# Performance work log

Measured on AMD Instinct MI355X. Metric: run time of the kernel, lower is better.

Reference implementation:

```python
import jax, jax.numpy as jnp
import numpy as np

NEG = -1.0e9
OBS_VOCAB = 64
Y_CLASSES = 32


def setup_inputs() -> dict:
    key = jax.random.key(0)
    ks = jax.random.split(key, 6)
    B, V, N, O, Y, HID = 256, 32, 8192, OBS_VOCAB, Y_CLASSES, 128
    tables = jax.random.randint(ks[0], (B, V, N), 0, O)
    sigma = jax.random.randint(ks[1], (B, N), 0, Y)
    x = jax.random.randint(ks[2], (B,), 0, N)
    base_obs = jax.random.randint(ks[3], (B,), 0, O)
    W1 = jax.random.normal(ks[4], (3, HID), dtype=jnp.float32) * 0.1
    b1 = jnp.zeros((HID,), dtype=jnp.float32)
    W2 = jax.random.normal(ks[5], (HID, 1), dtype=jnp.float32) * 0.1
    b2 = jnp.zeros((1,), dtype=jnp.float32)
    return {"tables": tables, "sigma": sigma, "x": x, "base_obs": base_obs,
            "W1": W1, "b1": b1, "W2": W2, "b2": b2, "max_steps": 8}


def reference(tables, sigma, x, base_obs, W1, b1, W2, b2, max_steps):
    B, V, N = tables.shape
    bidx = jnp.arange(B)
    vidx = jnp.arange(V)

    def step(carry, _):
        m, stopped, used = carry  # m: [B,N] candidate mask, used: [B,V]
        mf = m.astype(jnp.float32)
        total = jnp.maximum(mf.sum(-1), 1.0)  # [B]
        # oracle features: expected posterior set size after asking each view
        # counts[b,v,o] = #candidates in m whose tables[b,v,:] label is o
        counts = jnp.zeros((B, V, OBS_VOCAB), jnp.float32).at[
            bidx[:, None, None], vidx[None, :, None], tables].add(mf[:, None, :])
        gathered = jnp.take_along_axis(counts, tables, axis=-1)  # [B,V,N]
        exp_size = (gathered * mf[:, None, :]).sum(-1) / total[:, None]  # [B,V]
        steps_f = jnp.log2(jnp.maximum(exp_size, 1.0))
        amb_f = exp_size - 1.0
        feat_views = jnp.stack([steps_f, amb_f, exp_size], axis=-1)  # [B,V,3]
        feat_views = feat_views.at[:, 0, 0].set(1000.0)  # oracle cfg forbid_view0
        closed = total <= 1.0
        stop_steps = jnp.where(closed, 0.0, 1000.0)  # allow_stop_only_if_closed
        feat_stop = jnp.stack([stop_steps, total - 1.0, total], axis=-1)[:, None, :]
        feat = jnp.clip(jnp.concatenate([feat_views, feat_stop], axis=1), -1000.0, 1000.0)
        h = jax.nn.gelu(feat @ W1 + b1, approximate=False)
        z_logits = jax.lax.stop_gradient((h @ W2 + b2)[..., 0])  # [B,V+1] (detached)
        # straight-through z on detached logits reduces to a hard one-hot constant
        z = jax.nn.one_hot(jnp.argmax(z_logits, axis=-1), V + 1, dtype=jnp.float32)
        logits = z.at[:, 0].set(NEG)  # forbid view 0
        used_full = jnp.concatenate([used, jnp.zeros((B, 1), bool)], axis=1)
        logits = jnp.where(used_full, NEG, logits)  # mask already-used views
        a = jnp.argmax(logits, axis=-1)
        a = jnp.where(stopped, V, a)
        is_stop = a == V
        ac = jnp.clip(a, 0, V - 1)
        r = tables[bidx, ac, x]
        r = jnp.where(is_stop, 0, r)
        m_new = m & (is_stop[:, None] | (tables[bidx, ac, :] == r[:, None]))
        used_new = used.at[bidx, ac].set(True)
        return (m_new, stopped | is_stop, used_new), (a, r)

    m0 = tables[:, 0, :] == base_obs[:, None]
    carry0 = (m0, jnp.zeros((B,), bool), jnp.zeros((B, V), bool))
    (m, _, _), (a_seq, r_seq) = jax.lax.scan(step, carry0, None, length=int(max_steps))
    actions = a_seq.T  # [B, T]
    responses = r_seq.T
    # predict_y: exact constructive posterior over classes from candidate mask
    w = m.astype(jnp.float32)
    denom = jnp.maximum(w.sum(-1, keepdims=True), 1.0)
    state_dist = w / denom  # [B,N]
    p_sig = jnp.zeros((B, Y_CLASSES), jnp.float32).at[bidx[:, None], sigma].add(state_dist)
    y_logits = jnp.log(jnp.maximum(p_sig, 1e-9))
    return actions, responses, y_logits
```

## Files before the change

### kernel.cpp

```cpp
#include <hip/hip_runtime.h>
#include <math.h>

#define HP 65

__device__ __forceinline__ float clip1000(float v) {
  return fminf(fmaxf(v, -1000.0f), 1000.0f);
}

__device__ __noinline__ float mlp16(const float* w1a, const float* w1b,
                                    const float* w1c, const float* b1v,
                                    const float* w2v,
                                    float f0, float f1, float f2, int l) {
  float zp = 0.0f;
  {
    #pragma clang fp contract(off)
    #pragma clang loop unroll(disable)
    for (int k = l * 8; k < l * 8 + 8; ++k) {
      float pre = f0 * w1a[k] + f1 * w1b[k] + f2 * w1c[k] + b1v[k];
      float e = erff(pre / (float)M_SQRT2);
      float hg = 0.5f * pre * (1.0f + e);
      zp = zp + hg * w2v[k];
    }
  }
  zp += __shfl_xor(zp, 1);
  zp += __shfl_xor(zp, 2);
  zp += __shfl_xor(zp, 4);
  zp += __shfl_xor(zp, 8);
  return zp;
}

__launch_bounds__(1024, 1)
__global__ void sim_kernel(const int* __restrict__ tables,
                           const int* __restrict__ sigma,
                           const int* __restrict__ x,
                           const int* __restrict__ base_obs,
                           const float* __restrict__ W1,
                           const float* __restrict__ b1,
                           const float* __restrict__ W2,
                           const float* __restrict__ b2,
                           const int* __restrict__ max_steps_p,
                           float* __restrict__ out,
                           int B, int V, int N)
{
  const int b = blockIdx.x;
  const int tid = threadIdx.x;
  const int T = max_steps_p[0];

  __shared__ unsigned short s_pos[8192];
  __shared__ int s_gidx[8192];
  __shared__ int s_lab[256 * 33];
  __shared__ int s_h[2][32 * HP];
  __shared__ int s_surv[256];
  __shared__ float s_w1a[128], s_w1b[128], s_w1c[128], s_b1v[128], s_w2v[128];
  __shared__ float s_z[33];
  __shared__ float s_zc[6];
  __shared__ int s_used[32];
  __shared__ int s_ycnt[32];
  __shared__ int s_resp[32];
  __shared__ float s_b2v;
  __shared__ int s_nact, s_cnt, s_a, s_r;

  const int* tb = tables + (size_t)b * V * N;
  const int* sg = sigma + (size_t)b * N;
  const int bo = base_obs[b];
  const int xb = x[b];

  if (tid < 128) s_w1a[tid] = W1[tid];
  else if (tid < 256) s_w1b[tid - 128] = W1[tid];
  else if (tid < 384) s_w1c[tid - 256] = W1[tid];
  else if (tid < 512) s_b1v[tid - 384] = b1[tid - 384];
  else if (tid < 640) s_w2v[tid - 512] = W2[tid - 512];
  else if (tid == 640) s_b2v = b2[0];
  else if (tid >= 704 && tid < 736) s_resp[tid - 704] = tb[(size_t)(tid - 704) * N + xb];
  #pragma clang loop unroll(disable)
  for (int i = tid; i < 2 * 32 * HP; i += 1024) ((int*)s_h)[i] = 0;
  if (tid < 32) { s_used[tid] = 0; s_ycnt[tid] = 0; }
  if (tid == 0) s_nact = 0;
  __syncthreads();

  if (tid < 928) {
    const int4* tb4 = (const int4*)tb;
    #pragma clang loop unroll(disable)
    for (int q = tid; q < (N >> 2); q += 928) {
      int4 v4 = tb4[q]; int base = q << 2;
      if (v4.x == bo) { int p = atomicAdd(&s_nact, 1); s_gidx[p] = base; }
      if (v4.y == bo) { int p = atomicAdd(&s_nact, 1); s_gidx[p] = base + 1; }
      if (v4.z == bo) { int p = atomicAdd(&s_nact, 1); s_gidx[p] = base + 2; }
      if (v4.w == bo) { int p = atomicAdd(&s_nact, 1); s_gidx[p] = base + 3; }
    }
  } else {
    const int g = (tid - 928) >> 4, l = (tid - 928) & 15;
    const float zcf[6][3] = {
      {1.0f, 1.0f, 2.0f},
      {0.0f, 0.0f, 1.0f},
      {1000.0f, 0.0f, 1.0f},
      {1000.0f, 1.0f, 2.0f},
      {0.0f, -1.0f, 0.0f},
      {1000.0f, -1.0f, 0.0f}};
    if (g < 6) {
      float zp = mlp16(s_w1a, s_w1b, s_w1c, s_b1v, s_w2v,
                       zcf[g][0], zcf[g][1], zcf[g][2], l);
      if (l == 0) s_zc[g] = zp + s_b2v;
    }
  }
  __syncthreads();

  const int nact0 = s_nact;
  const bool cached = (nact0 <= 256);
  const int v32 = tid >> 5, g32 = tid & 31;

  auto labelOf = [&](int pos, int vv) -> int {
    return cached ? s_lab[pos * 33 + vv] : tb[(size_t)vv * N + s_gidx[pos]];
  };

  {
    const int* row = tb + (size_t)v32 * N;
    if (cached) {
      int labs[8];
      #pragma unroll
      for (int u = 0; u < 8; ++u) {
        int j = g32 + (u << 5);
        if (j < nact0) labs[u] = row[s_gidx[j]];
      }
      #pragma unroll
      for (int u = 0; u < 8; ++u) {
        int j = g32 + (u << 5);
        if (j < nact0) {
          s_lab[j * 33 + v32] = labs[u];
          atomicAdd(&s_h[0][v32 * HP + labs[u]], 1);
        }
      }
    } else {
      #pragma clang loop unroll(disable)
      for (int j = g32; j < nact0; j += 32)
        atomicAdd(&s_h[0][v32 * HP + row[s_gidx[j]]], 1);
    }
    #pragma clang loop unroll(disable)
    for (int j = tid; j < nact0; j += 1024) s_pos[j] = (unsigned short)j;
  }
  __syncthreads();

  int t = 0; bool stopped = false, tail = false; int hc = 0;
  while (t < T) {
    const int nact = s_nact;
    if (nact <= 2) { tail = true; break; }

    if (tid < 528) {
      const int view = tid >> 4, l = tid & 15;
      const float total = (float)nact;
      float f0, f1, f2;
      if (view == 32) {
        f0 = 1000.0f;
        f1 = clip1000(total - 1.0f);
        f2 = clip1000(total);
      } else {
        long long sumsq = 0;
        #pragma unroll
        for (int o = l * 4; o < l * 4 + 4; ++o) {
          long long c = (long long)s_h[hc][view * HP + o];
          sumsq += c * c;
        }
        sumsq += __shfl_xor(sumsq, 1);
        sumsq += __shfl_xor(sumsq, 2);
        sumsq += __shfl_xor(sumsq, 4);
        sumsq += __shfl_xor(sumsq, 8);
        float es = (float)sumsq / total;
        float steps = (view == 0) ? 1000.0f : log2f(fmaxf(es, 1.0f));
        f0 = clip1000(steps); f1 = clip1000(es - 1.0f); f2 = clip1000(es);
      }
      float zp = mlp16(s_w1a, s_w1b, s_w1c, s_b1v, s_w2v, f0, f1, f2, l);
      if (l == 0) s_z[view] = zp + s_b2v;
    } else if (tid >= 544) {
      #pragma clang loop unroll(disable)
      for (int i = tid - 544; i < 32 * HP; i += 480) s_h[hc ^ 1][i] = 0;
    }
    __syncthreads();

    if (tid == 0) {
      int jstar = 0; float best = s_z[0];
      #pragma clang loop unroll(disable)
      for (int i = 1; i < 33; ++i) { float zz = s_z[i]; if (zz > best) { best = zz; jstar = i; } }
      int a;
      if (jstar == 32 || (jstar >= 1 && !s_used[jstar])) a = jstar;
      else {
        a = 32;
        #pragma clang loop unroll(disable)
        for (int i = 1; i < 32; ++i)
          if (!s_used[i]) { a = i; break; }
      }
      int r = 0;
      if (a != 32) { s_used[a] = 1; r = s_resp[a]; }
      s_a = a; s_r = r; s_cnt = 0;
      out[b * T + t] = (float)a;
      out[(size_t)B * T + b * T + t] = (float)r;
    }
    __syncthreads();

    const int a = s_a, r = s_r;
    if (a == 32) { stopped = true; break; }

    for (int c0 = 0; c0 < nact; c0 += 256) {
      int labs[8], poss[8];
      #pragma unroll
      for (int u = 0; u < 8; ++u) {
        int j = c0 + g32 + (u << 5);
        if (j < nact) { poss[u] = s_pos[j]; labs[u] = labelOf(poss[u], v32); }
      }
      if (v32 == a) {
        #pragma unroll
        for (int u = 0; u < 8; ++u) {
          int j = c0 + g32 + (u << 5);
          if (j < nact) s_surv[j - c0] = (labs[u] == r);
        }
      }
      __syncthreads();
      if (v32 == a) {
        #pragma unroll
        for (int u = 0; u < 8; ++u) {
          int j = c0 + g32 + (u << 5);
          if (j < nact && labs[u] == r) {
            int p = atomicAdd(&s_cnt, 1);
            s_pos[p] = (unsigned short)poss[u];
          }
        }
      }
      #pragma unroll
      for (int u = 0; u < 8; ++u) {
        int j = c0 + g32 + (u << 5);
        if (j < nact && s_surv[j - c0]) atomicAdd(&s_h[hc ^ 1][v32 * HP + labs[u]], 1);
      }
      __syncthreads();
    }
    if (tid == 0) s_nact = s_cnt;
    hc ^= 1;
    ++t;
    __syncthreads();
  }

  if (stopped && tid == 0) {
    #pragma clang loop unroll(disable)
    for (int tt = t + 1; tt < T; ++tt) {
      out[b * T + tt] = (float)V;
      out[(size_t)B * T + b * T + tt] = 0.0f;
    }
  }

  if (tail) {
    if (tid < 64) {
      const int lane = tid;
      int nact = s_nact;
      int p0 = (nact >= 1) ? (int)s_pos[0] : 0;
      int p1 = (nact == 2) ? (int)s_pos[1] : 0;
      unsigned usedmask;
      { bool ub = (lane < 32) && (s_used[lane] != 0);
        usedmask = (unsigned)__ballot(ub); }
      const float zA = s_zc[0], zB = s_zc[1], zC = s_zc[2],
                  zD = s_zc[3], zE = s_zc[4], zF = s_zc[5];
      unsigned esmask = 0;
      if (nact == 2) {
        int l0 = (lane < 32) ? labelOf(p0, lane) : 0;
        int l1 = (lane < 32) ? labelOf(p1, lane) : 0;
        esmask = (unsigned)__ballot(lane < 32 && (l0 == l1));
      }

      #pragma clang loop unroll(disable)
      for (; t < T; ++t) {
        int jstar; float best;
        if (nact == 2) {
          best = (esmask & 1u) ? zD : zC; jstar = 0;
          #pragma clang loop unroll(disable)
          for (int i = 1; i < 32; ++i) {
            float zz = ((esmask >> i) & 1u) ? zA : zB;
            if (zz > best) { best = zz; jstar = i; }
          }
          if (zD > best) { best = zD; jstar = 32; }
        } else if (nact == 1) {
          best = zC; jstar = 0;
          if (zB > best) { best = zB; jstar = 1; }
        } else {
          best = zF; jstar = 0;
          if (zE > best) { best = zE; jstar = 1; }
          if (zB > best) { best = zB; jstar = 32; }
        }
        int a;
        if (jstar == 32 || (jstar >= 1 && !((usedmask >> jstar) & 1u))) a = jstar;
        else {
          unsigned freeb = ~usedmask & 0x7ffffffeu;
          a = freeb ? (int)__builtin_ctz(freeb) : 32;
        }
        if (a == 32) {
          if (lane == 0) {
            #pragma clang loop unroll(disable)
            for (int tt = t; tt < T; ++tt) {
              out[b * T + tt] = (float)V;
              out[(size_t)B * T + b * T + tt] = 0.0f;
            }
          }
          break;
        }
        usedmask |= (1u << a);
        int r = s_resp[a];
        if (lane == 0) {
          out[b * T + t] = (float)a;
          out[(size_t)B * T + b * T + t] = (float)r;
        }
        if (nact == 2) {
          bool k0 = (labelOf(p0, a) == r);
          bool k1 = (labelOf(p1, a) == r);
          if (k0 && k1) {  }
          else if (k0) { nact = 1; }
          else if (k1) { nact = 1; p0 = p1; }
          else { nact = 0; }
        } else if (nact == 1) {
          if (labelOf(p0, a) != r) nact = 0;
        }
      }
      if (lane == 0) {
        s_nact = nact;
        if (nact >= 1) s_pos[0] = (unsigned short)p0;
      }
    }
    __syncthreads();
  }

  const int nfin = s_nact;
  #pragma clang loop unroll(disable)
  for (int j = tid; j < nfin; j += 1024) {
    atomicAdd(&s_ycnt[sg[s_gidx[s_pos[j]]]], 1);
  }
  __syncthreads();
  if (tid < 32) {
    float denom = (float)(nfin > 1 ? nfin : 1);
    float q = 1.0f / denom;
    int c = s_ycnt[tid];
    float p = 0.0f;
    #pragma clang loop unroll(disable)
    for (int k = 0; k < c; ++k) p = p + q;
    out[(size_t)2 * B * T + b * 32 + tid] = logf(fmaxf(p, 1e-9f));
  }
}

extern "C" void kernel_launch(void* const* d_in, const int* in_sizes, int n_in,
                              void* d_out, int out_size, void* d_ws, size_t ws_size,
                              hipStream_t stream) {
  const int* tables   = (const int*)d_in[0];
  const int* sigma    = (const int*)d_in[1];
  const int* x        = (const int*)d_in[2];
  const int* base_obs = (const int*)d_in[3];
  const float* W1 = (const float*)d_in[4];
  const float* b1 = (const float*)d_in[5];
  const float* W2 = (const float*)d_in[6];
  const float* b2 = (const float*)d_in[7];
  const int* msteps = (const int*)d_in[8];
  float* out = (float*)d_out;

  const int B = in_sizes[2];
  const int N = in_sizes[1] / B;
  const int V = in_sizes[0] / (B * N);

  sim_kernel<<<dim3(B), dim3(1024), 0, stream>>>(
      tables, sigma, x, base_obs, W1, b1, W2, b2, msteps, out, B, V, N);
}
```

Baseline: 40.70 us.

## Restructure step loop into unified filter+histogram pass with double-buffered positions

Merges the initial histogram build and the per-step filter/histogram update into one loop body at the top of the while loop, with the survivor list double-buffered in two s_pos arrays. The histogram becomes single-buffered and is cleared before each pass, and the MLP weights are packed into one shared array. Loops that were fully unrolled with per-thread register arrays become non-unrolled strided loops, and labels are re-read from shared memory in the histogram phase. This trims register pressure and code size but adds an extra barrier and a serial clear per step.

```diff
diff --git a/kernel.cpp b/kernel.cpp
--- a/kernel.cpp
+++ b/kernel.cpp
@@ -7,10 +7,10 @@
   return fminf(fmaxf(v, -1000.0f), 1000.0f);
 }
 
-__device__ __noinline__ float mlp16(const float* w1a, const float* w1b,
-                                    const float* w1c, const float* b1v,
-                                    const float* w2v,
-                                    float f0, float f1, float f2, int l) {
+__device__ __noinline__ float mlp16(const float* sw, float f0, float f1, float f2, int l) {
+  const float* w1a = sw;        const float* w1b = sw + 128;
+  const float* w1c = sw + 256;  const float* b1v = sw + 384;
+  const float* w2v = sw + 512;
   float zp = 0.0f;
   {
     #pragma clang fp contract(off)
@@ -46,18 +46,15 @@
   const int tid = threadIdx.x;
   const int T = max_steps_p[0];
 
-  __shared__ unsigned short s_pos[8192];
+  __shared__ unsigned short s_pos[2][8192];
   __shared__ int s_gidx[8192];
   __shared__ int s_lab[256 * 33];
-  __shared__ int s_h[2][32 * HP];
+  __shared__ int s_h[32 * HP];
   __shared__ int s_surv[256];
-  __shared__ float s_w1a[128], s_w1b[128], s_w1c[128], s_b1v[128], s_w2v[128];
+  __shared__ float s_w[641];
   __shared__ float s_z[33];
   __shared__ float s_zc[6];
-  __shared__ int s_used[32];
-  __shared__ int s_ycnt[32];
-  __shared__ int s_resp[32];
-  __shared__ float s_b2v;
+  __shared__ int s_used[32], s_ycnt[32], s_resp[32];
   __shared__ int s_nact, s_cnt, s_a, s_r;
 
   const int* tb = tables + (size_t)b * V * N;
@@ -65,15 +62,15 @@
   const int bo = base_obs[b];
   const int xb = x[b];
 
-  if (tid < 128) s_w1a[tid] = W1[tid];
-  else if (tid < 256) s_w1b[tid - 128] = W1[tid];
-  else if (tid < 384) s_w1c[tid - 256] = W1[tid];
-  else if (tid < 512) s_b1v[tid - 384] = b1[tid - 384];
-  else if (tid < 640) s_w2v[tid - 512] = W2[tid - 512];
-  else if (tid == 640) s_b2v = b2[0];
-  else if (tid >= 704 && tid < 736) s_resp[tid - 704] = tb[(size_t)(tid - 704) * N + xb];
-  #pragma clang loop unroll(disable)
-  for (int i = tid; i < 2 * 32 * HP; i += 1024) ((int*)s_h)[i] = 0;
+  {
+    float wv = 0.0f;
+    if (tid < 384) wv = W1[tid];
+    else if (tid < 512) wv = b1[tid - 384];
+    else if (tid < 640) wv = W2[tid - 512];
+    else if (tid == 640) wv = b2[0];
+    if (tid <= 640) s_w[tid] = wv;
+  }
+  if (tid >= 704 && tid < 736) s_resp[tid - 704] = tb[(size_t)(tid - 704) * N + xb];
   if (tid < 32) { s_used[tid] = 0; s_ycnt[tid] = 0; }
   if (tid == 0) s_nact = 0;
   __syncthreads();
@@ -98,9 +95,8 @@
       {0.0f, -1.0f, 0.0f},
       {1000.0f, -1.0f, 0.0f}};
     if (g < 6) {
-      float zp = mlp16(s_w1a, s_w1b, s_w1c, s_b1v, s_w2v,
-                       zcf[g][0], zcf[g][1], zcf[g][2], l);
-      if (l == 0) s_zc[g] = zp + s_b2v;
+      float zp = mlp16(s_w, zcf[g][0], zcf[g][1], zcf[g][2], l);
+      if (l == 0) s_zc[g] = zp + s_w[640];
     }
   }
   __syncthreads();
@@ -108,46 +104,68 @@
   const int nact0 = s_nact;
   const bool cached = (nact0 <= 256);
   const int v32 = tid >> 5, g32 = tid & 31;
+  #pragma clang loop unroll(disable)
+  for (int j = tid; j < nact0; j += 1024) s_pos[0][j] = (unsigned short)j;
 
   auto labelOf = [&](int pos, int vv) -> int {
     return cached ? s_lab[pos * 33 + vv] : tb[(size_t)vv * N + s_gidx[pos]];
   };
 
-  {
-    const int* row = tb + (size_t)v32 * N;
-    if (cached) {
-      int labs[8];
-      #pragma unroll
-      for (int u = 0; u < 8; ++u) {
-        int j = g32 + (u << 5);
-        if (j < nact0) labs[u] = row[s_gidx[j]];
-      }
-      #pragma unroll
-      for (int u = 0; u < 8; ++u) {
-        int j = g32 + (u << 5);
-        if (j < nact0) {
-          s_lab[j * 33 + v32] = labs[u];
-          atomicAdd(&s_h[0][v32 * HP + labs[u]], 1);
-        }
-      }
-    } else {
+  int cur = 0, t = 0, a = -1, r = 0;
+  bool first = true, stopped = false, tail = false;
+
+  while (true) {
+    const bool need_hist = (t < T);
+    const int nact = s_nact;
+
+    if (need_hist) {
       #pragma clang loop unroll(disable)
-      for (int j = g32; j < nact0; j += 32)
-        atomicAdd(&s_h[0][v32 * HP + row[s_gidx[j]]], 1);
-    }
-    #pragma clang loop unroll(disable)
-    for (int j = tid; j < nact0; j += 1024) s_pos[j] = (unsigned short)j;
-  }
-  __syncthreads();
-
-  int t = 0; bool stopped = false, tail = false; int hc = 0;
-  while (t < T) {
-    const int nact = s_nact;
-    if (nact <= 2) { tail = true; break; }
+      for (int i = tid; i < 32 * HP; i += 1024) s_h[i] = 0;
+    }
+    if (tid == 0) s_cnt = 0;
+    __syncthreads();
+    for (int c0 = 0; c0 < nact; c0 += 256) {
+      const int cend = (nact < c0 + 256) ? nact : c0 + 256;
+      if (first || v32 == a) {
+        #pragma clang loop unroll(disable)
+        for (int j = c0 + g32; j < cend; j += 32) {
+          int pos = s_pos[cur][j];
+          int lab;
+          if (first) {
+            lab = tb[(size_t)v32 * N + s_gidx[pos]];
+            if (cached) s_lab[pos * 33 + v32] = lab;
+          } else {
+            lab = labelOf(pos, v32);
+          }
+          if (a >= 0 && v32 == a) {
+            int sv = (lab == r);
+            s_surv[j - c0] = sv;
+            if (sv) { int p = atomicAdd(&s_cnt, 1); s_pos[cur ^ 1][p] = (unsigned short)pos; }
+          }
+        }
+      }
+      __syncthreads();
+      if (cend >= nact && tid == 0 && a >= 0) s_nact = s_cnt;
+      if (need_hist) {
+        #pragma clang loop unroll(disable)
+        for (int j = c0 + g32; j < cend; j += 32) {
+          if (a < 0 || s_surv[j - c0]) {
+            int pos = s_pos[cur][j];
+            atomicAdd(&s_h[v32 * HP + labelOf(pos, v32)], 1);
+          }
+        }
+      }
+      __syncthreads();
+    }
+    if (a >= 0) cur ^= 1;
+    first = false;
+
+    if (s_nact <= 2) { tail = true; break; }
+    if (t >= T) break;
 
     if (tid < 528) {
       const int view = tid >> 4, l = tid & 15;
-      const float total = (float)nact;
+      const float total = (float)s_nact;
       float f0, f1, f2;
       if (view == 32) {
         f0 = 1000.0f;
@@ -155,9 +173,9 @@
         f2 = clip1000(total);
       } else {
         long long sumsq = 0;
-        #pragma unroll
+        #pragma clang loop unroll(disable)
         for (int o = l * 4; o < l * 4 + 4; ++o) {
-          long long c = (long long)s_h[hc][view * HP + o];
+          long long c = (long long)s_h[view * HP + o];
           sumsq += c * c;
         }
         sumsq += __shfl_xor(sumsq, 1);
@@ -168,11 +186,8 @@
         float steps = (view == 0) ? 1000.0f : log2f(fmaxf(es, 1.0f));
         f0 = clip1000(steps); f1 = clip1000(es - 1.0f); f2 = clip1000(es);
       }
-      float zp = mlp16(s_w1a, s_w1b, s_w1c, s_b1v, s_w2v, f0, f1, f2, l);
-      if (l == 0) s_z[view] = zp + s_b2v;
-    } else if (tid >= 544) {
-      #pragma clang loop unroll(disable)
-      for (int i = tid - 544; i < 32 * HP; i += 480) s_h[hc ^ 1][i] = 0;
+      float zp = mlp16(s_w, f0, f1, f2, l);
+      if (l == 0) s_z[view] = zp + s_w[640];
     }
     __syncthreads();
 
@@ -180,66 +195,29 @@
       int jstar = 0; float best = s_z[0];
       #pragma clang loop unroll(disable)
       for (int i = 1; i < 33; ++i) { float zz = s_z[i]; if (zz > best) { best = zz; jstar = i; } }
-      int a;
-      if (jstar == 32 || (jstar >= 1 && !s_used[jstar])) a = jstar;
+      int aa;
+      if (jstar == 32 || (jstar >= 1 && !s_used[jstar])) aa = jstar;
       else {
-        a = 32;
+        aa = 32;
         #pragma clang loop unroll(disable)
         for (int i = 1; i < 32; ++i)
-          if (!s_used[i]) { a = i; break; }
-      }
-      int r = 0;
-      if (a != 32) { s_used[a] = 1; r = s_resp[a]; }
-      s_a = a; s_r = r; s_cnt = 0;
-      out[b * T + t] = (float)a;
-      out[(size_t)B * T + b * T + t] = (float)r;
+          if (!s_used[i]) { aa = i; break; }
+      }
+      int rr = 0;
+      if (aa != 32) { s_used[aa] = 1; rr = s_resp[aa]; }
+      s_a = aa; s_r = rr;
+      out[b * T + t] = (float)aa;
+      out[(size_t)B * T + b * T + t] = (float)rr;
     }
     __syncthreads();
-
-    const int a = s_a, r = s_r;
+    a = s_a; r = s_r;
+    ++t;
     if (a == 32) { stopped = true; break; }
-
-    for (int c0 = 0; c0 < nact; c0 += 256) {
-      int labs[8], poss[8];
-      #pragma unroll
-      for (int u = 0; u < 8; ++u) {
-        int j = c0 + g32 + (u << 5);
-        if (j < nact) { poss[u] = s_pos[j]; labs[u] = labelOf(poss[u], v32); }
-      }
-      if (v32 == a) {
-        #pragma unroll
-        for (int u = 0; u < 8; ++u) {
-          int j = c0 + g32 + (u << 5);
-          if (j < nact) s_surv[j - c0] = (labs[u] == r);
-        }
-      }
-      __syncthreads();
-      if (v32 == a) {
-        #pragma unroll
-        for (int u = 0; u < 8; ++u) {
-          int j = c0 + g32 + (u << 5);
-          if (j < nact && labs[u] == r) {
-            int p = atomicAdd(&s_cnt, 1);
-            s_pos[p] = (unsigned short)poss[u];
-          }
-        }
-      }
-      #pragma unroll
-      for (int u = 0; u < 8; ++u) {
-        int j = c0 + g32 + (u << 5);
-        if (j < nact && s_surv[j - c0]) atomicAdd(&s_h[hc ^ 1][v32 * HP + labs[u]], 1);
-      }
-      __syncthreads();
-    }
-    if (tid == 0) s_nact = s_cnt;
-    hc ^= 1;
-    ++t;
-    __syncthreads();
   }
 
   if (stopped && tid == 0) {
     #pragma clang loop unroll(disable)
-    for (int tt = t + 1; tt < T; ++tt) {
+    for (int tt = t; tt < T; ++tt) {
       out[b * T + tt] = (float)V;
       out[(size_t)B * T + b * T + tt] = 0.0f;
     }
@@ -249,8 +227,8 @@
     if (tid < 64) {
       const int lane = tid;
       int nact = s_nact;
-      int p0 = (nact >= 1) ? (int)s_pos[0] : 0;
-      int p1 = (nact == 2) ? (int)s_pos[1] : 0;
+      int p0 = (nact >= 1) ? (int)s_pos[cur][0] : 0;
+      int p1 = (nact == 2) ? (int)s_pos[cur][1] : 0;
       unsigned usedmask;
       { bool ub = (lane < 32) && (s_used[lane] != 0);
         usedmask = (unsigned)__ballot(ub); }
@@ -282,13 +260,13 @@
           if (zE > best) { best = zE; jstar = 1; }
           if (zB > best) { best = zB; jstar = 32; }
         }
-        int a;
-        if (jstar == 32 || (jstar >= 1 && !((usedmask >> jstar) & 1u))) a = jstar;
+        int a2;
+        if (jstar == 32 || (jstar >= 1 && !((usedmask >> jstar) & 1u))) a2 = jstar;
         else {
           unsigned freeb = ~usedmask & 0x7ffffffeu;
-          a = freeb ? (int)__builtin_ctz(freeb) : 32;
-        }
-        if (a == 32) {
+          a2 = freeb ? (int)__builtin_ctz(freeb) : 32;
+        }
+        if (a2 == 32) {
           if (lane == 0) {
             #pragma clang loop unroll(disable)
             for (int tt = t; tt < T; ++tt) {
@@ -298,26 +276,26 @@
           }
           break;
         }
-        usedmask |= (1u << a);
-        int r = s_resp[a];
+        usedmask |= (1u << a2);
+        int r2 = s_resp[a2];
         if (lane == 0) {
-          out[b * T + t] = (float)a;
-          out[(size_t)B * T + b * T + t] = (float)r;
+          out[b * T + t] = (float)a2;
+          out[(size_t)B * T + b * T + t] = (float)r2;
         }
         if (nact == 2) {
-          bool k0 = (labelOf(p0, a) == r);
-          bool k1 = (labelOf(p1, a) == r);
+          bool k0 = (labelOf(p0, a2) == r2);
+          bool k1 = (labelOf(p1, a2) == r2);
           if (k0 && k1) {  }
           else if (k0) { nact = 1; }
           else if (k1) { nact = 1; p0 = p1; }
           else { nact = 0; }
         } else if (nact == 1) {
-          if (labelOf(p0, a) != r) nact = 0;
+          if (labelOf(p0, a2) != r2) nact = 0;
         }
       }
       if (lane == 0) {
         s_nact = nact;
-        if (nact >= 1) s_pos[0] = (unsigned short)p0;
+        if (nact >= 1) s_pos[cur][0] = (unsigned short)p0;
       }
     }
     __syncthreads();
@@ -326,7 +304,7 @@
   const int nfin = s_nact;
   #pragma clang loop unroll(disable)
   for (int j = tid; j < nfin; j += 1024) {
-    atomicAdd(&s_ycnt[sg[s_gidx[s_pos[j]]]], 1);
+    atomicAdd(&s_ycnt[sg[s_gidx[s_pos[cur][j]]]], 1);
   }
   __syncthreads();
   if (tid < 32) {
```

After: 42.12 us. 1.03x slower.
